# Performance work log

Measured on AMD Instinct MI355X. Metric: run time of the kernel, lower is better.

The kernel has to match this reference:

```python
import jax, jax.numpy as jnp
import numpy as np


def setup_inputs() -> dict:
    key = jax.random.key(0)
    x = jax.random.normal(key, (32, 64, 64, 64), dtype=jnp.float32)
    return {"x": x, "num_zeros": 2}


def reference(x, num_zeros):
    # ZeroWeave: interleave `num_zeros` zeros between every pair of pixels
    # along both spatial dims (equivalent to the gather_nd over
    # concat([x, zeros_like(x)]) with the precomputed index tensor).
    # x: [B, C, H, W] -> [B, C, H*s - num_zeros, W*s - num_zeros], s = num_zeros + 1
    s = num_zeros + 1
    B, C, H, W = x.shape
    out_h = H * s - num_zeros
    out_w = W * s - num_zeros
    out = jnp.zeros((B, C, out_h, out_w), dtype=x.dtype)
    out = out.at[:, :, ::s, ::s].set(x)
    return out
```

## Files before the change

### kernel.cpp

```cpp
#include <hip/hip_runtime.h>


typedef float vfloat4 __attribute__((ext_vector_type(4)));

constexpr int PLANE_IN   = 64 * 64;
constexpr int PLANE_OUT4 = 190 * 190 / 4;
constexpr int GROUP4     = 285;
constexpr int NPLANES    = 32 * 64;
constexpr int BLOCK      = 256;
constexpr int FULL_ITERS = PLANE_OUT4 / BLOCK;
constexpr int TAIL       = PLANE_OUT4 - FULL_ITERS * BLOCK;

__global__ __launch_bounds__(BLOCK) void ZeroWeave_89601607729830_kernel(
    const float* __restrict__ x, float* __restrict__ out) {
    __shared__ float    xs[PLANE_IN];
    __shared__ unsigned tab[GROUP4];

    const int bc = blockIdx.x;
    const int t  = threadIdx.x;

    {
        const vfloat4* xp = reinterpret_cast<const vfloat4*>(x + bc * PLANE_IN);
        vfloat4* xl = reinterpret_cast<vfloat4*>(xs);
#pragma unroll
        for (int k = 0; k < PLANE_IN / 4 / BLOCK; ++k)
            xl[k * BLOCK + t] = __builtin_nontemporal_load(xp + k * BLOCK + t);
    }

    for (int p = t; p < GROUP4; p += BLOCK) {
        unsigned packed = 0;
#pragma unroll
        for (int j = 0; j < 4; ++j) {
            unsigned e  = 4u * p + j;
            unsigned h  = (e * 44151u) >> 23;
            unsigned w  = e - h * 190u;
            unsigned h3 = (h * 171u) >> 9;
            unsigned hm = h - h3 * 3u;
            unsigned w3 = (w * 171u) >> 9;
            unsigned wm = w - w3 * 3u;
            unsigned src = ((hm | wm) == 0u) ? (h3 * 64u + w3) : 255u;
            packed |= src << (8 * j);
        }
        tab[p] = packed;
    }
    __syncthreads();

    vfloat4* op = reinterpret_cast<vfloat4*>(out) + bc * PLANE_OUT4;

    auto emit = [&](int q) {
        unsigned g      = ((unsigned)q * 58868u) >> 24;
        unsigned p      = (unsigned)q - g * 285u;
        unsigned xbase  = g << 7;
        unsigned packed = tab[p];
        vfloat4 v;
#pragma unroll
        for (int j = 0; j < 4; ++j) {
            unsigned b = (packed >> (8 * j)) & 255u;
            float val  = xs[(xbase + b) & (PLANE_IN - 1)];
            v[j] = (b != 255u) ? val : 0.0f;
        }
        __builtin_nontemporal_store(v, op + q);
    };

    for (int pass = 0; pass < 2; ++pass) {
#pragma unroll 4
        for (int k = 0; k < FULL_ITERS; ++k)
            emit(k * BLOCK + t);
        if (t < TAIL)
            emit(FULL_ITERS * BLOCK + t);
        __syncthreads();
    }
}

extern "C" void kernel_launch(void* const* d_in, const int* in_sizes, int n_in,
                              void* d_out, int out_size, void* d_ws, size_t ws_size,
                              hipStream_t stream) {
    const float* x = (const float*)d_in[0];
    float* out = (float*)d_out;

    ZeroWeave_89601607729830_kernel<<<NPLANES, BLOCK, 0, stream>>>(x, out);
}
```

Measured before the change: 403.1 us.

## Process four planes per block with register prefetch and double-buffered LDS

Each block now handles four input planes instead of one. While it emits the current plane from one LDS buffer, it prefetches the next plane into registers and then stores it into the other LDS buffer. The index table is built once per block and reused across the four planes. The earlier loop that wrote every output plane twice is gone, which removes half of the global store traffic. The trade-offs are a quarter as many blocks, more LDS per block and more registers held by the prefetch.

```diff
diff --git a/kernel.cpp b/kernel.cpp
--- a/kernel.cpp
+++ b/kernel.cpp
@@ -6,26 +6,20 @@
 constexpr int PLANE_IN   = 64 * 64;
 constexpr int PLANE_OUT4 = 190 * 190 / 4;
 constexpr int GROUP4     = 285;
-constexpr int NPLANES    = 32 * 64;
 constexpr int BLOCK      = 256;
+constexpr int PPB        = 4;
+constexpr int GRID       = (32 * 64) / PPB;
 constexpr int FULL_ITERS = PLANE_OUT4 / BLOCK;
 constexpr int TAIL       = PLANE_OUT4 - FULL_ITERS * BLOCK;
+constexpr int STAGE_VEC  = PLANE_IN / 4 / BLOCK;
 
 __global__ __launch_bounds__(BLOCK) void ZeroWeave_89601607729830_kernel(
     const float* __restrict__ x, float* __restrict__ out) {
-    __shared__ float    xs[PLANE_IN];
+    __shared__ float    xs[2][PLANE_IN];
     __shared__ unsigned tab[GROUP4];
 
-    const int bc = blockIdx.x;
-    const int t  = threadIdx.x;
-
-    {
-        const vfloat4* xp = reinterpret_cast<const vfloat4*>(x + bc * PLANE_IN);
-        vfloat4* xl = reinterpret_cast<vfloat4*>(xs);
-#pragma unroll
-        for (int k = 0; k < PLANE_IN / 4 / BLOCK; ++k)
-            xl[k * BLOCK + t] = __builtin_nontemporal_load(xp + k * BLOCK + t);
-    }
+    const int t   = threadIdx.x;
+    const int bc0 = blockIdx.x * PPB;
 
     for (int p = t; p < GROUP4; p += BLOCK) {
         unsigned packed = 0;
@@ -43,32 +37,57 @@
         }
         tab[p] = packed;
     }
+
+    {
+        const vfloat4* xp = reinterpret_cast<const vfloat4*>(x + bc0 * PLANE_IN);
+        vfloat4* xl = reinterpret_cast<vfloat4*>(xs[0]);
+#pragma unroll
+        for (int k = 0; k < STAGE_VEC; ++k)
+            xl[k * BLOCK + t] = __builtin_nontemporal_load(xp + k * BLOCK + t);
+    }
     __syncthreads();
 
-    vfloat4* op = reinterpret_cast<vfloat4*>(out) + bc * PLANE_OUT4;
+    for (int p = 0; p < PPB; ++p) {
+        vfloat4 pf[STAGE_VEC];
+        if (p + 1 < PPB) {
+            const vfloat4* xp =
+                reinterpret_cast<const vfloat4*>(x + (bc0 + p + 1) * PLANE_IN);
+#pragma unroll
+            for (int k = 0; k < STAGE_VEC; ++k)
+                pf[k] = __builtin_nontemporal_load(xp + k * BLOCK + t);
+        }
 
-    auto emit = [&](int q) {
-        unsigned g      = ((unsigned)q * 58868u) >> 24;
-        unsigned p      = (unsigned)q - g * 285u;
-        unsigned xbase  = g << 7;
-        unsigned packed = tab[p];
-        vfloat4 v;
+        const float* xsp = xs[p & 1];
+        vfloat4* op = reinterpret_cast<vfloat4*>(out) + (bc0 + p) * PLANE_OUT4;
+
+        auto emit = [&](int q) {
+            unsigned g      = ((unsigned)q * 58868u) >> 24;
+            unsigned pp     = (unsigned)q - g * 285u;
+            unsigned xbase  = g << 7;
+            unsigned packed = tab[pp];
+            vfloat4 v;
 #pragma unroll
-        for (int j = 0; j < 4; ++j) {
-            unsigned b = (packed >> (8 * j)) & 255u;
-            float val  = xs[(xbase + b) & (PLANE_IN - 1)];
-            v[j] = (b != 255u) ? val : 0.0f;
-        }
-        __builtin_nontemporal_store(v, op + q);
-    };
+            for (int j = 0; j < 4; ++j) {
+                unsigned b = (packed >> (8 * j)) & 255u;
+                float val  = xsp[(xbase + b) & (PLANE_IN - 1)];
+                v[j] = (b != 255u) ? val : 0.0f;
+            }
+            __builtin_nontemporal_store(v, op + q);
+        };
 
-    for (int pass = 0; pass < 2; ++pass) {
 #pragma unroll 4
         for (int k = 0; k < FULL_ITERS; ++k)
             emit(k * BLOCK + t);
         if (t < TAIL)
             emit(FULL_ITERS * BLOCK + t);
-        __syncthreads();
+
+        if (p + 1 < PPB) {
+            vfloat4* xl = reinterpret_cast<vfloat4*>(xs[(p + 1) & 1]);
+#pragma unroll
+            for (int k = 0; k < STAGE_VEC; ++k)
+                xl[k * BLOCK + t] = pf[k];
+            __syncthreads();
+        }
     }
 }
 
@@ -78,5 +97,5 @@
     const float* x = (const float*)d_in[0];
     float* out = (float*)d_out;
 
-    ZeroWeave_89601607729830_kernel<<<NPLANES, BLOCK, 0, stream>>>(x, out);
+    ZeroWeave_89601607729830_kernel<<<GRID, BLOCK, 0, stream>>>(x, out);
 }
```

Result: faster. 331.1 us (-17.9%).
